# Performance work log

Hardware: AMD Instinct MI355X
Metric: run time of the kernel (lower is better)

The kernel has to match this reference:

```python
import jax, jax.numpy as jnp
import numpy as np

N, E, D, H, L = 20000, 320000, 128, 8, 3
C = D // H  # per-head channels = 16


def setup_inputs() -> dict:
    key = jax.random.key(0)
    ks = jax.random.split(key, 20)
    s = 1.0 / np.sqrt(D)
    inp = {
        "x": jax.random.normal(ks[0], (N, D), dtype=jnp.float32),
        "edge_index": jax.random.randint(ks[1], (2, E), 0, N, dtype=jnp.int64),
        "Wq": jax.random.normal(ks[2], (L, D, D), dtype=jnp.float32) * s,
        "bq": jnp.zeros((L, D), dtype=jnp.float32),
        "Wk": jax.random.normal(ks[3], (L, D, D), dtype=jnp.float32) * s,
        "bk": jnp.zeros((L, D), dtype=jnp.float32),
        "Wv": jax.random.normal(ks[4], (L, D, D), dtype=jnp.float32) * s,
        "bv": jnp.zeros((L, D), dtype=jnp.float32),
        "Wskip": jax.random.normal(ks[5], (L, D, D), dtype=jnp.float32) * s,
        "bskip": jnp.zeros((L, D), dtype=jnp.float32),
        "Wbeta": jax.random.normal(ks[6], (L, 3 * D, 1), dtype=jnp.float32) * (1.0 / np.sqrt(3 * D)),
        "ln_g": jnp.ones((L, D), dtype=jnp.float32),
        "ln_b": jnp.zeros((L, D), dtype=jnp.float32),
        "Wout": jax.random.normal(ks[7], (D, D), dtype=jnp.float32) * s,
        "bout": jnp.zeros((D,), dtype=jnp.float32),
    }
    return inp


def _layer_norm(x, g, b, eps=1e-5):
    mu = jnp.mean(x, axis=-1, keepdims=True)
    var = jnp.mean(jnp.square(x - mu), axis=-1, keepdims=True)
    return (x - mu) * jax.lax.rsqrt(var + eps) * g + b


def _transformer_conv(x, src, dst, Wq, bq, Wk, bk, Wv, bv, Wskip, bskip, Wbeta):
    # project q/k/v: [N, D] -> [N, H, C]
    q = (x @ Wq + bq).reshape(N, H, C)
    k = (x @ Wk + bk).reshape(N, H, C)
    v = (x @ Wv + bv).reshape(N, H, C)
    # per-edge attention logits: [E, H]
    alpha = jnp.sum(q[dst] * k[src], axis=-1) / np.sqrt(C)
    # scatter-softmax over edges grouped by dst node
    m = jax.ops.segment_max(alpha, dst, num_segments=N)  # [N, H]
    m = jnp.where(jnp.isfinite(m), m, 0.0)
    ea = jnp.exp(alpha - m[dst])
    denom = jax.ops.segment_sum(ea, dst, num_segments=N)  # [N, H]
    attn = ea / (denom[dst] + 1e-16)  # [E, H]
    # weighted message aggregation: [N, H, C] -> [N, D]
    out = jax.ops.segment_sum(attn[:, :, None] * v[src], dst, num_segments=N)
    out = out.reshape(N, D)
    # beta-gated skip connection (beta=True, root_weight=True)
    x_r = x @ Wskip + bskip
    beta = jax.nn.sigmoid(jnp.concatenate([out, x_r, out - x_r], axis=-1) @ Wbeta)  # [N, 1]
    return beta * x_r + (1.0 - beta) * out


def reference(x, edge_index, Wq, bq, Wk, bk, Wv, bv, Wskip, bskip, Wbeta, ln_g, ln_b, Wout, bout):
    src, dst = edge_index[0], edge_index[1]
    for i in range(L):
        residual = x
        x = _transformer_conv(x, src, dst, Wq[i], bq[i], Wk[i], bk[i], Wv[i], bv[i],
                              Wskip[i], bskip[i], Wbeta[i])
        x = jax.nn.relu(x)  # dropout is identity in eval mode
        x = _layer_norm(x + residual, ln_g[i], ln_b[i])
    return x @ Wout + bout
```

## Files before the change

kernel.cpp:

```cpp
#include <hip/hip_runtime.h>

#define N_NODES 20000
#define N_EDGES 320000
#define DIM 128
#define NLAYER 3
#define SCAN_BLK 1024
#define N_SCAN_BLKS ((N_NODES + SCAN_BLK - 1) / SCAN_BLK)
#define LDS_STRIDE 136

#define PREP_CASTW_BLKS 208
#define PREP_ZERO_BLKS 79
#define PREP_TOTAL (PREP_CASTW_BLKS + PREP_ZERO_BLKS)

typedef __attribute__((ext_vector_type(8))) short short8;
typedef __attribute__((ext_vector_type(4))) float f32x4;
typedef __attribute__((ext_vector_type(2))) float f32x2;

__device__ inline ushort f2bf(float f) {
  uint u = __float_as_uint(f);
  uint r = (u + 0x7fffu + ((u >> 16) & 1u)) >> 16;
  return (ushort)r;
}
__device__ inline float bf2f(ushort u) { return __uint_as_float(((uint)u) << 16); }

__device__ inline uint f2fp8(float f) {
  return __builtin_amdgcn_cvt_pk_fp8_f32(f, 0.f, 0, false) & 0xffu;
}
__device__ inline void fp8x4_to_f32(uint w, float* o) {
  f32x2 lo = __builtin_amdgcn_cvt_pk_f32_fp8(w, false);
  f32x2 hi = __builtin_amdgcn_cvt_pk_f32_fp8(w, true);
  o[0] = lo[0]; o[1] = lo[1]; o[2] = hi[0]; o[3] = hi[1];
}

__global__ __launch_bounds__(256) void prep_kernel(
    const float* __restrict__ Wq, const float* __restrict__ Wk,
    const float* __restrict__ Wv, const float* __restrict__ Ws,
    const float* __restrict__ Wo, ushort* __restrict__ wt,
    int* __restrict__ degc, int* __restrict__ bsum) {
  int b = blockIdx.x;
  int t = threadIdx.x;
  if (b < PREP_CASTW_BLKS) {
    int z = b >> 4;
    int r = b & 15;
    int k0 = (r >> 2) * 32, n0 = (r & 3) * 32;
    const float* src;
    if (z < 12) {
      int l = z >> 2, j = z & 3;
      src = (j == 0 ? Wq : j == 1 ? Wk : j == 2 ? Wv : Ws) + (size_t)l * DIM * DIM;
    } else {
      src = Wo;
    }
    __shared__ float tile[32][33];
    int tx = t & 31, ty = t >> 5;
    #pragma unroll
    for (int i = 0; i < 32; i += 8)
      tile[ty + i][tx] = src[(size_t)(k0 + ty + i) * DIM + n0 + tx];
    __syncthreads();
    ushort* dst = wt + (size_t)z * DIM * DIM;
    #pragma unroll
    for (int i = 0; i < 32; i += 8)
      dst[(size_t)(n0 + ty + i) * DIM + k0 + tx] = f2bf(tile[tx][ty + i]);
  } else {
    int i = (b - PREP_CASTW_BLKS) * 256 + t;
    if (i < N_NODES) degc[i] = 0;
    else if (i < N_NODES + N_SCAN_BLKS) bsum[i - N_NODES] = 0;
  }
}


__global__ void count_deg_kernel(const int* __restrict__ ei, int* __restrict__ deg) {
  int e = blockIdx.x * 256 + threadIdx.x;
  if (e < N_EDGES) atomicAdd(&deg[ei[N_EDGES + e]], 1);
}

__global__ __launch_bounds__(SCAN_BLK) void scan_lookback_kernel(
    int* __restrict__ degc, int* __restrict__ rowptr, int* __restrict__ bsum) {
  __shared__ int wsum[16];
  __shared__ int prevs;
  int t = threadIdx.x, lane = t & 63, w = t >> 6, bid = blockIdx.x;
  int i = bid * SCAN_BLK + t;
  int val = (i < N_NODES) ? degc[i] : 0;
  if (i < N_NODES) degc[i] = 0;
  int s = val;
  #pragma unroll
  for (int off = 1; off < 64; off <<= 1) {
    int u = __shfl_up(s, off);
    if (lane >= off) s += u;
  }
  if (lane == 63) wsum[w] = s;
  __syncthreads();
  if (t < 16) {
    int wv = wsum[t];
    int ss = wv;
    #pragma unroll
    for (int off = 1; off < 16; off <<= 1) {
      int u = __shfl_up(ss, off);
      if (t >= off) ss += u;
    }
    wsum[t] = ss - wv;
  }
  __syncthreads();
  int excl = wsum[w] + s - val;
  if (t == SCAN_BLK - 1)
    __hip_atomic_store(&bsum[bid], excl + val + 1, __ATOMIC_RELEASE,
                       __HIP_MEMORY_SCOPE_AGENT);
  if (w == 0) {
    int p = 0;
    for (int j = lane; j < bid; j += 64) {
      int v;
      do {
        v = __hip_atomic_load(&bsum[j], __ATOMIC_ACQUIRE, __HIP_MEMORY_SCOPE_AGENT);
      } while (v == 0);
      p += v - 1;
    }
    #pragma unroll
    for (int off = 1; off < 64; off <<= 1) p += __shfl_xor(p, off);
    if (t == 0) prevs = p;
  }
  __syncthreads();
  int off0 = prevs;
  if (i < N_NODES) rowptr[i] = off0 + excl;
  if (bid == N_SCAN_BLKS - 1 && t == SCAN_BLK - 1) rowptr[N_NODES] = off0 + excl + val;
}

__global__ void scatter_kernel(const int* __restrict__ ei, const int* __restrict__ rowptr,
                               int* __restrict__ cursor, int* __restrict__ csr_src) {
  int e = blockIdx.x * 256 + threadIdx.x;
  if (e < N_EDGES) {
    int d = ei[N_EDGES + e];
    int s = ei[e];
    int pos = atomicAdd(&cursor[d], 1);
    csr_src[rowptr[d] + pos] = s;
  }
}

template <int IN_F32>
__global__ __launch_bounds__(512) void gemm_mfma_kernel(
    const void* __restrict__ Xp, const ushort* __restrict__ WT,
    const float* __restrict__ B0, const float* __restrict__ B1,
    const float* __restrict__ B2, const float* __restrict__ B3,
    void* __restrict__ O0, void* __restrict__ O1, void* __restrict__ O2,
    void* __restrict__ O3, int m0, int m1, int m2, int m3) {
  __shared__ ushort As[128 * LDS_STRIDE];
  int mat = blockIdx.y;
  const ushort* Wt = WT + (size_t)mat * DIM * DIM;
  const float* bias;
  void* O;
  int mode;
  switch (mat) {
    case 0: bias = B0; O = O0; mode = m0; break;
    case 1: bias = B1; O = O1; mode = m1; break;
    case 2: bias = B2; O = O2; mode = m2; break;
    default: bias = B3; O = O3; mode = m3; break;
  }
  int t = threadIdx.x;
  int wid = t >> 6, lane = t & 63;
  int row0 = blockIdx.x * 128;
  int wr = wid >> 1, wc = wid & 1;
  int lr = lane & 15;
  int kc8 = (lane >> 4) * 8;

  if (IN_F32) {
    const float* Xf = (const float*)Xp;
    int rowi = t >> 5;
    int col4 = (t & 31) * 4;
    #pragma unroll
    for (int pass = 0; pass < 8; ++pass) {
      int row = pass * 16 + rowi;
      int gr = min(row0 + row, N_NODES - 1);
      float4 f = *(const float4*)(Xf + (size_t)gr * DIM + col4);
      ushort4 u;
      u.x = f2bf(f.x); u.y = f2bf(f.y); u.z = f2bf(f.z); u.w = f2bf(f.w);
      *(ushort4*)(As + row * LDS_STRIDE + col4) = u;
    }
  } else {
    const ushort* X = (const ushort*)Xp;
    int rowi = t >> 4;
    int col = (t & 15) * 8;
    #pragma unroll
    for (int pass = 0; pass < 4; ++pass) {
      int row = pass * 32 + rowi;
      int gr = min(row0 + row, N_NODES - 1);
      short8 val = *(const short8*)(X + (size_t)gr * DIM + col);
      *(short8*)(As + row * LDS_STRIDE + col) = val;
    }
  }
  __syncthreads();

  f32x4 acc[2][4];
  #pragma unroll
  for (int i = 0; i < 2; ++i)
    #pragma unroll
    for (int j = 0; j < 4; ++j) acc[i][j] = (f32x4){0.f, 0.f, 0.f, 0.f};

  #pragma unroll
  for (int ks = 0; ks < 4; ++ks) {
    short8 b[4];
    #pragma unroll
    for (int cf = 0; cf < 4; ++cf) {
      int c = wc * 64 + cf * 16 + lr;
      b[cf] = *(const short8*)(Wt + (size_t)c * DIM + ks * 32 + kc8);
    }
    #pragma unroll
    for (int rf = 0; rf < 2; ++rf) {
      int r = wr * 32 + rf * 16 + lr;
      short8 a = *(const short8*)(As + r * LDS_STRIDE + ks * 32 + kc8);
      #pragma unroll
      for (int cf = 0; cf < 4; ++cf)
        acc[rf][cf] = __builtin_amdgcn_mfma_f32_16x16x32_bf16(a, b[cf], acc[rf][cf], 0, 0, 0);
    }
  }

  #pragma unroll
  for (int cf = 0; cf < 4; ++cf) {
    int c = wc * 64 + cf * 16 + lr;
    float bv = bias[c];
    #pragma unroll
    for (int rf = 0; rf < 2; ++rf) {
      #pragma unroll
      for (int reg = 0; reg < 4; ++reg) {
        int r = row0 + wr * 32 + rf * 16 + (lane >> 4) * 4 + reg;
        if (r < N_NODES) {
          float val = acc[rf][cf][reg] + bv;
          if (mode == 0)
            ((ushort*)O)[(size_t)r * DIM + c] = f2bf(val);
          else if (mode == 1)
            ((float*)O)[(size_t)r * DIM + c] = val;
          else if (mode == 2)
            ((unsigned char*)O)[(size_t)r * 256 + c] = (unsigned char)f2fp8(val);
          else
            ((unsigned char*)O)[(size_t)r * 256 + 128 + c] = (unsigned char)f2fp8(val);
        }
      }
    }
  }
}

template <int RES_F32>
__global__ __launch_bounds__(256) void attn_fused_kernel(
    const ushort* __restrict__ q, const unsigned char* __restrict__ kv,
    const ushort* __restrict__ xr, const void* __restrict__ xres,
    const int* __restrict__ rowptr, const int* __restrict__ csr_src,
    const float* __restrict__ wbeta, const float* __restrict__ lng,
    const float* __restrict__ lnb, ushort* __restrict__ xnextb) {
  __shared__ float red[4][8][8][20];
  int w = threadIdx.x >> 6;
  int lane = threadIdx.x & 63;
  int n = blockIdx.x * 4 + w;
  int h = lane & 7, e = lane >> 3;

  const ushort* qrow = q + (size_t)n * DIM + h * 16;
  short8 q0 = *(const short8*)qrow;
  short8 q1 = *(const short8*)(qrow + 8);
  float qf[16];
  #pragma unroll
  for (int i = 0; i < 8; ++i) {
    qf[i] = bf2f((ushort)q0[i]) * 0.25f;
    qf[8 + i] = bf2f((ushort)q1[i]) * 0.25f;
  }

  int s0 = rowptr[n];
  int deg = rowptr[n + 1] - s0;
  int dm1 = deg - 1;
  float acc[16];
  #pragma unroll
  for (int i = 0; i < 16; ++i) acc[i] = 0.f;
  float dsum = 0.f;

  for (int base = 0; base < deg; base += 16) {
    int i1 = base + e, i2 = base + 8 + e;
    bool va1 = i1 < deg, va2 = i2 < deg;
    int src1 = csr_src[s0 + min(i1, dm1)];
    int src2 = csr_src[s0 + min(i2, dm1)];
    const unsigned char* r1 = kv + (size_t)src1 * 256 + h * 16;
    const unsigned char* r2 = kv + (size_t)src2 * 256 + h * 16;
    uint4 ku1 = *(const uint4*)r1;
    uint4 vu1 = *(const uint4*)(r1 + 128);
    uint4 ku2 = *(const uint4*)r2;
    uint4 vu2 = *(const uint4*)(r2 + 128);
    float kf[16], vf[16];
    fp8x4_to_f32(ku1.x, kf + 0); fp8x4_to_f32(ku1.y, kf + 4);
    fp8x4_to_f32(ku1.z, kf + 8); fp8x4_to_f32(ku1.w, kf + 12);
    fp8x4_to_f32(vu1.x, vf + 0); fp8x4_to_f32(vu1.y, vf + 4);
    fp8x4_to_f32(vu1.z, vf + 8); fp8x4_to_f32(vu1.w, vf + 12);
    float p = 0.f;
    #pragma unroll
    for (int i = 0; i < 16; ++i) p = fmaf(qf[i], kf[i], p);
    float ea = va1 ? __expf(p) : 0.f;
    dsum += ea;
    #pragma unroll
    for (int i = 0; i < 16; ++i) acc[i] = fmaf(ea, vf[i], acc[i]);
    fp8x4_to_f32(ku2.x, kf + 0); fp8x4_to_f32(ku2.y, kf + 4);
    fp8x4_to_f32(ku2.z, kf + 8); fp8x4_to_f32(ku2.w, kf + 12);
    fp8x4_to_f32(vu2.x, vf + 0); fp8x4_to_f32(vu2.y, vf + 4);
    fp8x4_to_f32(vu2.z, vf + 8); fp8x4_to_f32(vu2.w, vf + 12);
    p = 0.f;
    #pragma unroll
    for (int i = 0; i < 16; ++i) p = fmaf(qf[i], kf[i], p);
    ea = va2 ? __expf(p) : 0.f;
    dsum += ea;
    #pragma unroll
    for (int i = 0; i < 16; ++i) acc[i] = fmaf(ea, vf[i], acc[i]);
  }

  {
    float* my = &red[w][e][h][0];
    *(float4*)(my + 0) = make_float4(acc[0], acc[1], acc[2], acc[3]);
    *(float4*)(my + 4) = make_float4(acc[4], acc[5], acc[6], acc[7]);
    *(float4*)(my + 8) = make_float4(acc[8], acc[9], acc[10], acc[11]);
    *(float4*)(my + 12) = make_float4(acc[12], acc[13], acc[14], acc[15]);
    my[16] = dsum;
  }
  asm volatile("s_waitcnt lgkmcnt(0)" ::: "memory");

  int c0 = lane * 2;
  int hh = lane >> 3, cc = (lane & 7) * 2;
  float o0 = 0.f, o1 = 0.f, den = 0.f;
  #pragma unroll
  for (int ee = 0; ee < 8; ++ee) {
    float2 tv = *(float2*)&red[w][ee][hh][cc];
    o0 += tv.x;
    o1 += tv.y;
    den += red[w][ee][hh][16];
  }
  float inv = 1.f / (den + 1e-16f);
  o0 *= inv;
  o1 *= inv;

  ushort2 xru = *(const ushort2*)(xr + (size_t)n * DIM + c0);
  float xr0 = bf2f(xru.x), xr1 = bf2f(xru.y);
  float wa0 = wbeta[c0] + wbeta[2 * DIM + c0];
  float wa1 = wbeta[c0 + 1] + wbeta[2 * DIM + c0 + 1];
  float wb0 = wbeta[DIM + c0] - wbeta[2 * DIM + c0];
  float wb1 = wbeta[DIM + c0 + 1] - wbeta[2 * DIM + c0 + 1];
  float bs = o0 * wa0 + o1 * wa1 + xr0 * wb0 + xr1 * wb1;
  #pragma unroll
  for (int off = 1; off < 64; off <<= 1) bs += __shfl_xor(bs, off);
  float beta = 1.f / (1.f + __expf(-bs));
  float y0 = fmaxf(beta * xr0 + (1.f - beta) * o0, 0.f);
  float y1 = fmaxf(beta * xr1 + (1.f - beta) * o1, 0.f);
  float rv0, rv1;
  if (RES_F32) {
    float2 rv = *(const float2*)((const float*)xres + (size_t)n * DIM + c0);
    rv0 = rv.x; rv1 = rv.y;
  } else {
    ushort2 ru = *(const ushort2*)((const ushort*)xres + (size_t)n * DIM + c0);
    rv0 = bf2f(ru.x); rv1 = bf2f(ru.y);
  }
  y0 += rv0;
  y1 += rv1;
  float s = y0 + y1;
  #pragma unroll
  for (int off = 1; off < 64; off <<= 1) s += __shfl_xor(s, off);
  float mu = s * (1.f / 128.f);
  float d0 = y0 - mu, d1 = y1 - mu;
  float vs = d0 * d0 + d1 * d1;
  #pragma unroll
  for (int off = 1; off < 64; off <<= 1) vs += __shfl_xor(vs, off);
  float rstd = rsqrtf(vs * (1.f / 128.f) + 1e-5f);
  float2 g = *(const float2*)(lng + c0);
  float2 b = *(const float2*)(lnb + c0);
  float out0 = d0 * rstd * g.x + b.x;
  float out1 = d1 * rstd * g.y + b.y;
  ushort2 ob;
  ob.x = f2bf(out0);
  ob.y = f2bf(out1);
  *(ushort2*)(xnextb + (size_t)n * DIM + c0) = ob;
}


extern "C" void kernel_launch(void* const* d_in, const int* in_sizes, int n_in,
                              void* d_out, int out_size, void* d_ws, size_t ws_size,
                              hipStream_t stream) {
  const float* x_in = (const float*)d_in[0];
  const int* ei = (const int*)d_in[1];
  const float* Wq = (const float*)d_in[2];
  const float* bq = (const float*)d_in[3];
  const float* Wk = (const float*)d_in[4];
  const float* bk = (const float*)d_in[5];
  const float* Wv = (const float*)d_in[6];
  const float* bv = (const float*)d_in[7];
  const float* Wsk = (const float*)d_in[8];
  const float* bsk = (const float*)d_in[9];
  const float* Wb = (const float*)d_in[10];
  const float* lng = (const float*)d_in[11];
  const float* lnb = (const float*)d_in[12];
  const float* Wout = (const float*)d_in[13];
  const float* bout = (const float*)d_in[14];
  float* out = (float*)d_out;

  char* p = (char*)d_ws;
  auto alloc = [&](size_t bytes) {
    char* r = p;
    p += (bytes + 255) & ~(size_t)255;
    return r;
  };
  const size_t NB2 = (size_t)N_NODES * DIM * 2;
  ushort* xbb = (ushort*)alloc(NB2);
  ushort* qb = (ushort*)alloc(NB2);
  unsigned char* kvb = (unsigned char*)alloc((size_t)N_NODES * 256);
  ushort* xrb = (ushort*)alloc(NB2);
  ushort* wt = (ushort*)alloc((size_t)13 * DIM * DIM * 2);
  int* rowptr = (int*)alloc((N_NODES + 1) * 4);
  int* degc = (int*)alloc(N_NODES * 4);
  int* bsum = (int*)alloc(N_SCAN_BLKS * 4);
  int* csr_src = (int*)alloc(N_EDGES * 4);

  prep_kernel<<<PREP_TOTAL, 256, 0, stream>>>(Wq, Wk, Wv, Wsk, Wout, wt, degc, bsum);
  count_deg_kernel<<<(N_EDGES + 255) / 256, 256, 0, stream>>>(ei, degc);
  scan_lookback_kernel<<<N_SCAN_BLKS, SCAN_BLK, 0, stream>>>(degc, rowptr, bsum);
  scatter_kernel<<<(N_EDGES + 255) / 256, 256, 0, stream>>>(ei, rowptr, degc, csr_src);

  const int GX = (N_NODES + 127) / 128;
  for (int l = 0; l < NLAYER; ++l) {
    if (l == 0) {
      gemm_mfma_kernel<1><<<dim3(GX, 4), 512, 0, stream>>>(
          (const void*)x_in, wt + (size_t)l * 4 * DIM * DIM,
          bq + (size_t)l * DIM, bk + (size_t)l * DIM, bv + (size_t)l * DIM,
          bsk + (size_t)l * DIM,
          qb, kvb, kvb, xrb, 0, 2, 3, 0);
      attn_fused_kernel<1><<<N_NODES / 4, 256, 0, stream>>>(
          qb, kvb, xrb, (const void*)x_in, rowptr, csr_src,
          Wb + (size_t)l * 3 * DIM, lng + (size_t)l * DIM, lnb + (size_t)l * DIM,
          xbb);
    } else {
      gemm_mfma_kernel<0><<<dim3(GX, 4), 512, 0, stream>>>(
          (const void*)xbb, wt + (size_t)l * 4 * DIM * DIM,
          bq + (size_t)l * DIM, bk + (size_t)l * DIM, bv + (size_t)l * DIM,
          bsk + (size_t)l * DIM,
          qb, kvb, kvb, xrb, 0, 2, 3, 0);
      attn_fused_kernel<0><<<N_NODES / 4, 256, 0, stream>>>(
          qb, kvb, xrb, (const void*)xbb, rowptr, csr_src,
          Wb + (size_t)l * 3 * DIM, lng + (size_t)l * DIM, lnb + (size_t)l * DIM,
          xbb);
    }
  }
  gemm_mfma_kernel<0><<<dim3(GX, 1), 512, 0, stream>>>(
      (const void*)xbb, wt + (size_t)12 * DIM * DIM, bout, bout, bout, bout,
      out, out, out, out, 1, 1, 1, 1);
}
```

Baseline: 207.6 us.

## Halve GEMM block threads with larger per-wave tiles; prefetch CSR sources in attention loop

The GEMM kernel now runs 256 threads (4 waves) per block, with each wave computing a 64x64 output tile instead of 32x64. This reuses each loaded B fragment across more MFMAs at the cost of more accumulator registers. The attention gather loop now processes 8 edges per iteration instead of 16, with one K/V record in flight per lane instead of two, and software-prefetches the next csr_src index. The intent is to cut register pressure and hide index-load latency, but it may lose memory-level parallelism in the gather.

```diff
diff --git a/kernel.cpp b/kernel.cpp
--- a/kernel.cpp
+++ b/kernel.cpp
@@ -135,7 +135,7 @@
 }
 
 template <int IN_F32>
-__global__ __launch_bounds__(512) void gemm_mfma_kernel(
+__global__ __launch_bounds__(256) void gemm_mfma_kernel(
     const void* __restrict__ Xp, const ushort* __restrict__ WT,
     const float* __restrict__ B0, const float* __restrict__ B1,
     const float* __restrict__ B2, const float* __restrict__ B3,
@@ -165,8 +165,8 @@
     int rowi = t >> 5;
     int col4 = (t & 31) * 4;
     #pragma unroll
-    for (int pass = 0; pass < 8; ++pass) {
-      int row = pass * 16 + rowi;
+    for (int pass = 0; pass < 16; ++pass) {
+      int row = pass * 8 + rowi;
       int gr = min(row0 + row, N_NODES - 1);
       float4 f = *(const float4*)(Xf + (size_t)gr * DIM + col4);
       ushort4 u;
@@ -178,8 +178,8 @@
     int rowi = t >> 4;
     int col = (t & 15) * 8;
     #pragma unroll
-    for (int pass = 0; pass < 4; ++pass) {
-      int row = pass * 32 + rowi;
+    for (int pass = 0; pass < 8; ++pass) {
+      int row = pass * 16 + rowi;
       int gr = min(row0 + row, N_NODES - 1);
       short8 val = *(const short8*)(X + (size_t)gr * DIM + col);
       *(short8*)(As + row * LDS_STRIDE + col) = val;
@@ -187,9 +187,9 @@
   }
   __syncthreads();
 
-  f32x4 acc[2][4];
-  #pragma unroll
-  for (int i = 0; i < 2; ++i)
+  f32x4 acc[4][4];
+  #pragma unroll
+  for (int i = 0; i < 4; ++i)
     #pragma unroll
     for (int j = 0; j < 4; ++j) acc[i][j] = (f32x4){0.f, 0.f, 0.f, 0.f};
 
@@ -202,8 +202,8 @@
       b[cf] = *(const short8*)(Wt + (size_t)c * DIM + ks * 32 + kc8);
     }
     #pragma unroll
-    for (int rf = 0; rf < 2; ++rf) {
-      int r = wr * 32 + rf * 16 + lr;
+    for (int rf = 0; rf < 4; ++rf) {
+      int r = wr * 64 + rf * 16 + lr;
       short8 a = *(const short8*)(As + r * LDS_STRIDE + ks * 32 + kc8);
       #pragma unroll
       for (int cf = 0; cf < 4; ++cf)
@@ -216,10 +216,10 @@
     int c = wc * 64 + cf * 16 + lr;
     float bv = bias[c];
     #pragma unroll
-    for (int rf = 0; rf < 2; ++rf) {
+    for (int rf = 0; rf < 4; ++rf) {
       #pragma unroll
       for (int reg = 0; reg < 4; ++reg) {
-        int r = row0 + wr * 32 + rf * 16 + (lane >> 4) * 4 + reg;
+        int r = row0 + wr * 64 + rf * 16 + (lane >> 4) * 4 + reg;
         if (r < N_NODES) {
           float val = acc[rf][cf][reg] + bv;
           if (mode == 0)
@@ -261,43 +261,35 @@
 
   int s0 = rowptr[n];
   int deg = rowptr[n + 1] - s0;
-  int dm1 = deg - 1;
   float acc[16];
   #pragma unroll
   for (int i = 0; i < 16; ++i) acc[i] = 0.f;
   float dsum = 0.f;
 
-  for (int base = 0; base < deg; base += 16) {
-    int i1 = base + e, i2 = base + 8 + e;
-    bool va1 = i1 < deg, va2 = i2 < deg;
-    int src1 = csr_src[s0 + min(i1, dm1)];
-    int src2 = csr_src[s0 + min(i2, dm1)];
-    const unsigned char* r1 = kv + (size_t)src1 * 256 + h * 16;
-    const unsigned char* r2 = kv + (size_t)src2 * 256 + h * 16;
-    uint4 ku1 = *(const uint4*)r1;
-    uint4 vu1 = *(const uint4*)(r1 + 128);
-    uint4 ku2 = *(const uint4*)r2;
-    uint4 vu2 = *(const uint4*)(r2 + 128);
+  int src_n = (deg > 0) ? csr_src[s0 + min(e, deg - 1)] : 0;
+  for (int base = 0; base < deg; base += 8) {
+    int idx = base + e;
+    bool valid = idx < deg;
+    int src = src_n;
+    if (base + 8 < deg)
+      src_n = csr_src[s0 + min(base + 8 + e, deg - 1)];
+    const unsigned char* rec = kv + (size_t)src * 256 + h * 16;
+    uint4 ku = *(const uint4*)rec;
+    uint4 vu = *(const uint4*)(rec + 128);
     float kf[16], vf[16];
-    fp8x4_to_f32(ku1.x, kf + 0); fp8x4_to_f32(ku1.y, kf + 4);
-    fp8x4_to_f32(ku1.z, kf + 8); fp8x4_to_f32(ku1.w, kf + 12);
-    fp8x4_to_f32(vu1.x, vf + 0); fp8x4_to_f32(vu1.y, vf + 4);
-    fp8x4_to_f32(vu1.z, vf + 8); fp8x4_to_f32(vu1.w, vf + 12);
+    fp8x4_to_f32(ku.x, kf + 0);
+    fp8x4_to_f32(ku.y, kf + 4);
+    fp8x4_to_f32(ku.z, kf + 8);
+    fp8x4_to_f32(ku.w, kf + 12);
+    fp8x4_to_f32(vu.x, vf + 0);
+    fp8x4_to_f32(vu.y, vf + 4);
+    fp8x4_to_f32(vu.z, vf + 8);
+    fp8x4_to_f32(vu.w, vf + 12);
     float p = 0.f;
     #pragma unroll
     for (int i = 0; i < 16; ++i) p = fmaf(qf[i], kf[i], p);
-    float ea = va1 ? __expf(p) : 0.f;
-    dsum += ea;
-    #pragma unroll
-    for (int i = 0; i < 16; ++i) acc[i] = fmaf(ea, vf[i], acc[i]);
-    fp8x4_to_f32(ku2.x, kf + 0); fp8x4_to_f32(ku2.y, kf + 4);
-    fp8x4_to_f32(ku2.z, kf + 8); fp8x4_to_f32(ku2.w, kf + 12);
-    fp8x4_to_f32(vu2.x, vf + 0); fp8x4_to_f32(vu2.y, vf + 4);
-    fp8x4_to_f32(vu2.z, vf + 8); fp8x4_to_f32(vu2.w, vf + 12);
-    p = 0.f;
-    #pragma unroll
-    for (int i = 0; i < 16; ++i) p = fmaf(qf[i], kf[i], p);
-    ea = va2 ? __expf(p) : 0.f;
+    float ea = __expf(p);
+    ea = valid ? ea : 0.f;
     dsum += ea;
     #pragma unroll
     for (int i = 0; i < 16; ++i) acc[i] = fmaf(ea, vf[i], acc[i]);
@@ -414,7 +406,7 @@
   const int GX = (N_NODES + 127) / 128;
   for (int l = 0; l < NLAYER; ++l) {
     if (l == 0) {
-      gemm_mfma_kernel<1><<<dim3(GX, 4), 512, 0, stream>>>(
+      gemm_mfma_kernel<1><<<dim3(GX, 4), 256, 0, stream>>>(
           (const void*)x_in, wt + (size_t)l * 4 * DIM * DIM,
           bq + (size_t)l * DIM, bk + (size_t)l * DIM, bv + (size_t)l * DIM,
           bsk + (size_t)l * DIM,
@@ -424,7 +416,7 @@
           Wb + (size_t)l * 3 * DIM, lng + (size_t)l * DIM, lnb + (size_t)l * DIM,
           xbb);
     } else {
-      gemm_mfma_kernel<0><<<dim3(GX, 4), 512, 0, stream>>>(
+      gemm_mfma_kernel<0><<<dim3(GX, 4), 256, 0, stream>>>(
           (const void*)xbb, wt + (size_t)l * 4 * DIM * DIM,
           bq + (size_t)l * DIM, bk + (size_t)l * DIM, bv + (size_t)l * DIM,
           bsk + (size_t)l * DIM,
@@ -435,7 +427,7 @@
           xbb);
     }
   }
-  gemm_mfma_kernel<0><<<dim3(GX, 1), 512, 0, stream>>>(
+  gemm_mfma_kernel<0><<<dim3(GX, 1), 256, 0, stream>>>(
       (const void*)xbb, wt + (size_t)12 * DIM * DIM, bout, bout, bout, bout,
       out, out, out, out, 1, 1, 1, 1);
 }
```

Result: faster. 193.0 us (median of 3 runs) (-7.0%).
